# Kernel optimization log

Hardware: AMD Instinct MI355X
Metric: run time of the kernel (lower is better)

The kernel has to match this reference:

```python
import jax, jax.numpy as jnp
import numpy as np
from jax import lax

EPS = 1e-5
S_CENTROIDS = 2048
K_NEIGH = 32


def _fps(xyz, S):
    """Farthest point sampling. xyz: (B,N,3) -> idx (B,S) int32."""
    B, N, _ = xyz.shape

    def body(carry, _):
        dist, farthest = carry  # (B,N), (B,)
        centroid = jnp.take_along_axis(xyz, farthest[:, None, None], axis=1)  # (B,1,3)
        d = jnp.sum((xyz - centroid) ** 2, axis=-1)  # (B,N)
        dist = jnp.minimum(dist, d)
        nxt = jnp.argmax(dist, axis=-1).astype(jnp.int32)
        return (dist, nxt), farthest

    init = (jnp.full((B, N), 1e10, xyz.dtype), jnp.zeros((B,), jnp.int32))
    _, idx = lax.scan(body, init, None, length=S)
    return idx.T  # (B,S)


def _knn(q, p, K):
    """q: (B,S,3) queries, p: (B,N,3) points -> idx (B,S,K) of K nearest."""
    d = (jnp.sum(q * q, -1)[:, :, None] + jnp.sum(p * p, -1)[:, None, :]
         - 2.0 * jnp.einsum('bsd,bnd->bsn', q, p))  # (B,S,N) sq dists
    _, idx = lax.top_k(-d, K)
    return idx


def _mlp_layer(x, w, g, b, m, v):
    # x: (B,S,K,Cin); 1x1 conv == channel matmul, then eval-mode BN, then ReLU
    x = jnp.einsum('bskc,oc->bsko', x, w)
    x = (x - m) * (g * lax.rsqrt(v + EPS)) + b
    return jax.nn.relu(x)


def setup_inputs() -> dict:
    key = jax.random.key(0)
    ks = jax.random.split(key, 8)
    B, N, D = 4, 8192, 64
    inp = {
        'xyz': jax.random.normal(ks[0], (B, N, 3), jnp.float32),
        'points': jax.random.normal(ks[1], (B, D, N), jnp.float32),
        'w0': jax.random.normal(ks[2], (64, 67), jnp.float32) * (1.0 / np.sqrt(67)),
        'g0': jnp.ones((64,), jnp.float32), 'b0': jnp.zeros((64,), jnp.float32),
        'm0': jnp.zeros((64,), jnp.float32), 'v0': jnp.ones((64,), jnp.float32),
        'w1': jax.random.normal(ks[3], (64, 64), jnp.float32) * (1.0 / np.sqrt(64)),
        'g1': jnp.ones((64,), jnp.float32), 'b1': jnp.zeros((64,), jnp.float32),
        'm1': jnp.zeros((64,), jnp.float32), 'v1': jnp.ones((64,), jnp.float32),
        'w2': jax.random.normal(ks[4], (128, 64), jnp.float32) * (1.0 / np.sqrt(64)),
        'g2': jnp.ones((128,), jnp.float32), 'b2': jnp.zeros((128,), jnp.float32),
        'm2': jnp.zeros((128,), jnp.float32), 'v2': jnp.ones((128,), jnp.float32),
    }
    return inp


def reference(xyz, points, w0, g0, b0, m0, v0, w1, g1, b1, m1, v1,
              w2, g2, b2, m2, v2):
    B, N, _ = xyz.shape
    S, K = S_CENTROIDS, K_NEIGH

    # FPS centroids (S < N path of the module)
    fps_idx = _fps(xyz, S)                                        # (B,S)
    new_xyz = jnp.take_along_axis(xyz, fps_idx[..., None], axis=1)  # (B,S,3)

    # KNN grouping
    idx = _knn(new_xyz, xyz, K)                                   # (B,S,K)
    grouped_xyz = jnp.take_along_axis(xyz[:, None], idx[..., None], axis=2)  # (B,S,K,3)
    grouped_xyz = grouped_xyz - new_xyz[:, :, None, :]

    # gather neighbor features: points (B,D,N) -> (B,N,D) -> (B,S,K,D)
    pts = jnp.transpose(points, (0, 2, 1))
    neigh = jnp.take_along_axis(pts[:, None], idx[..., None], axis=2)
    grouped = jnp.concatenate([grouped_xyz, neigh], axis=-1)      # (B,S,K,3+D)

    x = _mlp_layer(grouped, w0, g0, b0, m0, v0)
    x = _mlp_layer(x, w1, g1, b1, m1, v1)
    x = _mlp_layer(x, w2, g2, b2, m2, v2)                         # (B,S,K,128)

    new_points = jnp.transpose(jnp.max(x, axis=2), (0, 2, 1))     # (B,128,S)
    return new_xyz, new_points
```

## Files before the change

### kernel.cpp

```cpp
#include <hip/hip_runtime.h>
#include <cfloat>
#include <climits>

#define NPTS   8192
#define SCENT  2048
#define KNEIGH 32
#define BATCH  4
#define DFEAT  64
#define FPS_T  512
#define NV     8
#define NW     8
#define CAP    64
#define NCONS  252
#define CPB    63

typedef float v2f __attribute__((ext_vector_type(2)));

#define DPPTOP2(um, us, ctrl, rmask)                                                  \
    { unsigned _tm = (unsigned)__builtin_amdgcn_update_dpp(0, (int)(um), (ctrl),      \
                                                           (rmask), 0xf, false);     \
      unsigned _ts = (unsigned)__builtin_amdgcn_update_dpp(0, (int)(us), (ctrl),      \
                                                           (rmask), 0xf, false);     \
      unsigned _lo = ((um) < _tm) ? (um) : _tm;                                       \
      (us) = ((us) > _ts) ? (us) : _ts;                                               \
      (us) = ((us) > _lo) ? (us) : _lo;                                               \
      (um) = ((um) > _tm) ? (um) : _tm; }

#define FLUSH_PUB(Eidx, VX, VY, VZ, HASPREV, PX, PY, PZ)                              \
    if (((Eidx) & 63) == 63) {                                                        \
        const int base0 = (Eidx) - 63;                                                \
        if (t < 64 * 3) {                                                             \
            const int ci = base0 + t / 3;                                             \
            const int cc = t - (t / 3) * 3;                                           \
            float v;                                                                  \
            if (ci == (Eidx))                                                         \
                v = (cc == 0) ? (VX) : ((cc == 1) ? (VY) : (VZ));                     \
            else if ((HASPREV) && ci == (Eidx) - 1)                                   \
                v = (cc == 0) ? (PX) : ((cc == 1) ? (PY) : (PZ));                     \
            else                                                                      \
                v = (cc == 0) ? S.hx[ci] : ((cc == 1) ? S.hy[ci] : S.hz[ci]);         \
            __hip_atomic_store(&new_xyz[((size_t)b * SCENT + base0) * 3 + t], v,      \
                               __ATOMIC_RELAXED, __HIP_MEMORY_SCOPE_AGENT);           \
        }                                                                             \
        __syncthreads();                 \
        if (t == 0)                                                                   \
            __hip_atomic_store(&progress[b], (Eidx) + 1,                              \
                               __ATOMIC_RELEASE, __HIP_MEMORY_SCOPE_AGENT);           \
    }

struct FpsSh {
    float sx[NPTS], sy[NPTS], sz[NPTS];
    float hx[SCENT], hy[SCENT], hz[SCENT];
    alignas(16) unsigned slotQ[2][NW][4];
    int scand[CAP];
    int scnt;
    alignas(8) double sdd[2][NW];
    double sfv[NW];
    int sfo[NW];
};
struct ConsSh {
    float  spx[2048], spy[2048], spz[2048];
    double sp2[2048];
    float  tile[32 * 33];
    float  regA[64 * 68];
    float  regB[64 * 64];
    float  regC[128 * 64];
    float  prm[512];
};
union ShU { FpsSh f; ConsSh c; };

__global__ __launch_bounds__(FPS_T, 1) void fused_kernel(
        const float* __restrict__ xyz, float* __restrict__ new_xyz,
        const float* __restrict__ pts, float* __restrict__ ptsT,
        int* __restrict__ progress, int* __restrict__ tcount,
        float* __restrict__ out_points,
        const float* __restrict__ w0, const float* __restrict__ g0,
        const float* __restrict__ b0, const float* __restrict__ m0,
        const float* __restrict__ v0, const float* __restrict__ w1,
        const float* __restrict__ g1, const float* __restrict__ b1,
        const float* __restrict__ m1, const float* __restrict__ v1,
        const float* __restrict__ w2, const float* __restrict__ g2,
        const float* __restrict__ b2, const float* __restrict__ m2,
        const float* __restrict__ v2) {
    __shared__ ShU sh;
    const int t = threadIdx.x;
    const int lane = t & 63, w = t >> 6;

    if (blockIdx.x < BATCH) {
        FpsSh& S = sh.f;
        const int b = blockIdx.x;
        const float* X = xyz + (size_t)b * NPTS * 3;

        for (int p = t; p < NPTS; p += FPS_T) {
            S.sx[p] = X[3 * p + 0]; S.sy[p] = X[3 * p + 1]; S.sz[p] = X[3 * p + 2];
        }

        v2f px2[NV], py2[NV], pz2[NV], dist2[NV];
#pragma unroll
        for (int j = 0; j < NV; ++j) {
            int pA = t + FPS_T * j, pB = t + FPS_T * (j + NV);
            px2[j] = (v2f){X[3 * pA + 0], X[3 * pB + 0]};
            py2[j] = (v2f){X[3 * pA + 1], X[3 * pB + 1]};
            pz2[j] = (v2f){X[3 * pA + 2], X[3 * pB + 2]};
            dist2[j] = (v2f){1e10f, 1e10f};
        }
        float c0x = X[0], c0y = X[1], c0z = X[2];
        float c1x = 0.f, c1y = 0.f, c1z = 0.f;
        int dual = 0, buf = 0;
        int E = 1;
        if (t == 0) { S.hx[0] = c0x; S.hy[0] = c0y; S.hz[0] = c0z; }
        __syncthreads();

#pragma unroll 1
        while (true) {
            float m2s = -1.f, s2s = -1.f;
            {
                const v2f c0xx = {c0x, c0x}, c0yy = {c0y, c0y}, c0zz = {c0z, c0z};
                if (dual) {
                    const v2f c1xx = {c1x, c1x}, c1yy = {c1y, c1y}, c1zz = {c1z, c1z};
#pragma unroll
                    for (int j = 0; j < NV; ++j) {
                        v2f dx = px2[j] - c0xx, dy = py2[j] - c0yy, dz = pz2[j] - c0zz;
                        v2f d0 = __builtin_elementwise_fma(dx, dx,
                                 __builtin_elementwise_fma(dy, dy, dz * dz));
                        v2f ex = px2[j] - c1xx, ey = py2[j] - c1yy, ez = pz2[j] - c1zz;
                        v2f d1 = __builtin_elementwise_fma(ex, ex,
                                 __builtin_elementwise_fma(ey, ey, ez * ez));
                        v2f d  = __builtin_elementwise_min(d0, d1);
                        v2f nd = __builtin_elementwise_min(dist2[j], d);
                        dist2[j] = nd;
                        float hi = fmaxf(nd.x, nd.y), lo = fminf(nd.x, nd.y);
                        s2s = fmaxf(fmaxf(s2s, lo), fminf(m2s, hi));
                        m2s = fmaxf(m2s, hi);
                    }
                } else {
#pragma unroll
                    for (int j = 0; j < NV; ++j) {
                        v2f dx = px2[j] - c0xx, dy = py2[j] - c0yy, dz = pz2[j] - c0zz;
                        v2f d  = __builtin_elementwise_fma(dx, dx,
                                 __builtin_elementwise_fma(dy, dy, dz * dz));
                        v2f nd = __builtin_elementwise_min(dist2[j], d);
                        dist2[j] = nd;
                        float hi = fmaxf(nd.x, nd.y), lo = fminf(nd.x, nd.y);
                        s2s = fmaxf(fmaxf(s2s, lo), fminf(m2s, hi));
                        m2s = fmaxf(m2s, hi);
                    }
                }
            }
            const float m = m2s, sec = s2s;

            int mi = 0;
#pragma unroll
            for (int j = 0; j < NV; ++j) {
                mi = (dist2[j].x == m) ? (t + FPS_T * j)        : mi;
                mi = (dist2[j].y == m) ? (t + FPS_T * (j + NV)) : mi;
            }

            const unsigned myU = __float_as_uint(m);
            unsigned um = myU, us = __float_as_uint(sec);
            DPPTOP2(um, us, 0x111, 0xf);
            DPPTOP2(um, us, 0x112, 0xf);
            DPPTOP2(um, us, 0x114, 0xf);
            DPPTOP2(um, us, 0x118, 0xf);
            DPPTOP2(um, us, 0x142, 0xa);
            DPPTOP2(um, us, 0x143, 0xc);
            const unsigned wu  = (unsigned)__builtin_amdgcn_readlane((int)um, 63);
            const unsigned wsu = (unsigned)__builtin_amdgcn_readlane((int)us, 63);

            unsigned long long wb = __ballot(myU == wu);
            const int wl   = __ffsll(wb) - 1;
            const int widx = __builtin_amdgcn_readlane(mi, wl);
            const float thwf = __fmul_rn(__uint_as_float(wu), 0.999998f);
            unsigned long long b1m = __ballot(m >= thwf);
            unsigned long long b2m = __ballot(sec >= thwf);
            const unsigned tw = (b2m || __popcll(b1m) >= 2) ? 1u : 0u;
            if (lane == 0) {
                *(uint4*)&S.slotQ[buf][w][0] =
                    make_uint4(wu, (unsigned)widx | (tw << 14), wsu, 0u);
            }
            __syncthreads();

            unsigned mv[NW], mt4[NW], sv2[NW];
            {
                const uint4* qp = (const uint4*)&S.slotQ[buf][0][0];
                uint4 u0 = qp[0], u1 = qp[1], u2 = qp[2], u3 = qp[3];
                uint4 u4 = qp[4], u5 = qp[5], u6 = qp[6], u7 = qp[7];
                mv[0]=u0.x; mt4[0]=u0.y; sv2[0]=u0.z;
                mv[1]=u1.x; mt4[1]=u1.y; sv2[1]=u1.z;
                mv[2]=u2.x; mt4[2]=u2.y; sv2[2]=u2.z;
                mv[3]=u3.x; mt4[3]=u3.y; sv2[3]=u3.z;
                mv[4]=u4.x; mt4[4]=u4.y; sv2[4]=u4.z;
                mv[5]=u5.x; mt4[5]=u5.y; sv2[5]=u5.z;
                mv[6]=u6.x; mt4[6]=u6.y; sv2[6]=u6.z;
                mv[7]=u7.x; mt4[7]=u7.y; sv2[7]=u7.z;
            }
            unsigned gu = mv[0];
#pragma unroll
            for (int k = 1; k < NW; ++k) gu = (mv[k] > gu) ? mv[k] : gu;
            const float gvf  = __uint_as_float(gu);
            const float gthf = __fmul_rn(gvf, 0.999998f);
            const unsigned ugth = __float_as_uint(gthf);
            int nw = 0; unsigned meta = 0; int kw = 0;
#pragma unroll
            for (int k = NW - 1; k >= 0; --k) {
                nw  += (mv[k] >= ugth) ? 1 : 0;
                meta = (mv[k] == gu) ? mt4[k] : meta;
                kw   = (mv[k] == gu) ? k : kw;
            }
            const int wtie = (meta >> 14) & 1;
            int i1 = (int)(meta & 0x3fffu);
            const int fb = (nw >= 2) || wtie;

            if (fb) {
                if (t == 0) S.scnt = 0;
                __syncthreads();
#pragma unroll
                for (int j = 0; j < NV; ++j) {
                    if (dist2[j].x >= gthf) {
                        int slot = atomicAdd(&S.scnt, 1);
                        if (slot < CAP) S.scand[slot] = t + FPS_T * j;
                    }
                    if (dist2[j].y >= gthf) {
                        int slot = atomicAdd(&S.scnt, 1);
                        if (slot < CAP) S.scand[slot] = t + FPS_T * (j + NV);
                    }
                }
                __syncthreads();
                const int mm = S.scnt;
                if (mm <= CAP) {
                    double bd = -1.0; int bi = INT_MAX;
#pragma unroll 1
                    for (int k = 0; k < mm; ++k) {
                        const int pos = S.scand[k];
                        const double pxd = (double)S.sx[pos], pyd = (double)S.sy[pos],
                                     pzd = (double)S.sz[pos];
                        double dd = 1e10;
                        for (int i = t; i < E; i += FPS_T) {
                            double ddx = __dsub_rn(pxd, (double)S.hx[i]);
                            double ddy = __dsub_rn(pyd, (double)S.hy[i]);
                            double ddz = __dsub_rn(pzd, (double)S.hz[i]);
                            double d = __dadd_rn(__dadd_rn(__dmul_rn(ddx, ddx), __dmul_rn(ddy, ddy)),
                                                 __dmul_rn(ddz, ddz));
                            dd = fmin(dd, d);
                        }
#pragma unroll
                        for (int off = 32; off >= 1; off >>= 1)
                            dd = fmin(dd, __shfl_down(dd, off));
                        if (lane == 0) S.sdd[k & 1][w] = dd;
                        __syncthreads();
                        double ddm = S.sdd[k & 1][0];
#pragma unroll
                        for (int w2i = 1; w2i < NW; ++w2i) ddm = fmin(ddm, S.sdd[k & 1][w2i]);
                        if (ddm > bd || (ddm == bd && pos < bi)) { bd = ddm; bi = pos; }
                    }
                    i1 = bi;
                } else {
                    double bv = -1.0; int bi = INT_MAX;
#pragma unroll 1
                    for (int j = 0; j < 2 * NV; ++j) {
                        const int jj = j & (NV - 1);
                        const bool hiHalf = j >= NV;
                        const double pxd = (double)(hiHalf ? px2[jj].y : px2[jj].x);
                        const double pyd = (double)(hiHalf ? py2[jj].y : py2[jj].x);
                        const double pzd = (double)(hiHalf ? pz2[jj].y : pz2[jj].x);
                        double dd = 1e10;
                        for (int i = 0; i < E; ++i) {
                            double ddx = __dsub_rn(pxd, (double)S.hx[i]);
                            double ddy = __dsub_rn(pyd, (double)S.hy[i]);
                            double ddz = __dsub_rn(pzd, (double)S.hz[i]);
                            double d = __dadd_rn(__dadd_rn(__dmul_rn(ddx, ddx), __dmul_rn(ddy, ddy)),
                                                 __dmul_rn(ddz, ddz));
                            dd = fmin(dd, d);
                        }
                        int pidx = t + FPS_T * j;
                        if (dd > bv || (dd == bv && pidx < bi)) { bv = dd; bi = pidx; }
                    }
#pragma unroll
                    for (int off = 32; off >= 1; off >>= 1) {
                        double ov = __shfl_down(bv, off);
                        int    oi = __shfl_down(bi, off);
                        if (ov > bv || (ov == bv && oi < bi)) { bv = ov; bi = oi; }
                    }
                    if (lane == 0) { S.sfv[w] = bv; S.sfo[w] = bi; }
                    __syncthreads();
                    bv = S.sfv[0]; bi = S.sfo[0];
#pragma unroll
                    for (int w2i = 1; w2i < NW; ++w2i) {
                        double ov = S.sfv[w2i]; int oi = S.sfo[w2i];
                        if (ov > bv || (ov == bv && oi < bi)) { bv = ov; bi = oi; }
                    }
                    i1 = bi;
                }
                __syncthreads();
            }

            const float e0x = S.sx[i1], e0y = S.sy[i1], e0z = S.sz[i1];
            if (t == 0) { S.hx[E] = e0x; S.hy[E] = e0y; S.hz[E] = e0z; }
            FLUSH_PUB(E, e0x, e0y, e0z, 0, 0.f, 0.f, 0.f);
            c0x = e0x; c0y = e0y; c0z = e0z;

            int peeled = 0;
            float e1x = 0.f, e1y = 0.f, e1z = 0.f;
            if (!fb && (E + 1) < SCENT) {
                unsigned arr[NW];
#pragma unroll
                for (int k = 0; k < NW; ++k) arr[k] = (k == kw) ? sv2[k] : mv[k];
                unsigned v2u = arr[0];
#pragma unroll
                for (int k = 1; k < NW; ++k) v2u = (arr[k] > v2u) ? arr[k] : v2u;
                int k2 = 0; unsigned meta2 = 0;
#pragma unroll
                for (int k = NW - 1; k >= 0; --k) {
                    meta2 = (arr[k] == v2u) ? mt4[k] : meta2;
                    k2    = (arr[k] == v2u) ? k : k2;
                }
                const float v2vf = __uint_as_float(v2u);
                const unsigned uthr2 = __float_as_uint(__fmul_rn(v2vf, 0.999998f));
                int cnt = 0;
#pragma unroll
                for (int k = 0; k < NW; ++k)
                    cnt += ((mv[k] >= uthr2) ? 1 : 0) + ((sv2[k] >= uthr2) ? 1 : 0);
                const int i2 = (int)(meta2 & 0x3fffu);
                e1x = S.sx[i2]; e1y = S.sy[i2]; e1z = S.sz[i2];
                const float ddx = e1x - e0x, ddy = e1y - e0y, ddz = e1z - e0z;
                const float dq = fmaf(ddx, ddx, fmaf(ddy, ddy, ddz * ddz));
                peeled = ((k2 != kw) && (cnt == 2) &&
                          (dq >= __fmul_rn(v2vf, 1.000002f))) ? 1 : 0;
            }
            if (peeled) {
                const int e1i = E + 1;
                if (t == 0) { S.hx[e1i] = e1x; S.hy[e1i] = e1y; S.hz[e1i] = e1z; }
                FLUSH_PUB(e1i, e1x, e1y, e1z, 1, e0x, e0y, e0z);
                c1x = e1x; c1y = e1y; c1z = e1z;
                dual = 1;
                E = e1i + 1;
            } else {
                dual = 0;
                E = E + 1;
            }
            if (E >= SCENT) break;
            buf ^= 1;
        }
    } else {
        ConsSh& K = sh.c;
        const int local = blockIdx.x - BATCH;
        const int batch = local / CPB;
        const int cl    = local % CPB;
        const int tx = t & 31, ty = t >> 5;

        for (int tid2 = local; tid2 < 2048; tid2 += NCONS) {
            const int bt = tid2 >> 9, rest = tid2 & 511;
            const int d0 = (rest >> 8) * 32, n0 = (rest & 255) * 32;
            __syncthreads();
#pragma unroll
            for (int i = 0; i < 2; ++i)
                K.tile[(ty + 16 * i) * 33 + tx] =
                    pts[(size_t)bt * DFEAT * NPTS + (size_t)(d0 + ty + 16 * i) * NPTS + n0 + tx];
            __syncthreads();
#pragma unroll
            for (int i = 0; i < 2; ++i)
                ptsT[(size_t)bt * NPTS * DFEAT + (size_t)(n0 + ty + 16 * i) * DFEAT + d0 + tx] =
                    K.tile[tx * 33 + ty + 16 * i];
        }
        if (t == 0) {
            __threadfence();
            atomicAdd(tcount, 1);
        }

        for (int idx = t; idx < 64 * 68; idx += FPS_T) {
            int o = idx / 68, i = idx - o * 68;
            float v;
            if (i < 64)      v = w0[o * 67 + 3 + i];
            else if (i < 67) v = w0[o * 67 + (i - 64)];
            else             v = 0.0f;
            K.regA[idx] = v;
        }
        for (int idx = t; idx < 64 * 64; idx += FPS_T)  K.regB[idx] = w1[idx];
        for (int idx = t; idx < 128 * 64; idx += FPS_T) K.regC[idx] = w2[idx];
        if (t < 64) {
            float a0v = g0[t] / sqrtf(v0[t] + 1e-5f);
            K.prm[t]       = a0v;
            K.prm[64 + t]  = b0[t] - m0[t] * a0v;
            float a1v = g1[t] / sqrtf(v1[t] + 1e-5f);
            K.prm[128 + t] = a1v;
            K.prm[192 + t] = b1[t] - m1[t] * a1v;
        } else if (t < 192) {
            int o = t - 64;
            float a2v = g2[o] / sqrtf(v2[o] + 1e-5f);
            K.prm[256 + o] = a2v;
            K.prm[384 + o] = b2[o] - m2[o] * a2v;
        }

        const float* Xb = xyz + (size_t)batch * NPTS * 3;
#pragma unroll 1
        for (int r = 0; ; ++r) {
            const int sBase = r * (CPB * NW) + cl * NW;
            if (sBase >= SCENT) break;
            const int sMax = min(sBase + NW - 1, SCENT - 1);
            if (t == 0) {
                while (__hip_atomic_load(&progress[batch], __ATOMIC_ACQUIRE,
                                         __HIP_MEMORY_SCOPE_AGENT) < sMax + 1)
                    __builtin_amdgcn_s_sleep(8);
                if (r == 0) {
                    while (__hip_atomic_load(tcount, __ATOMIC_ACQUIRE,
                                             __HIP_MEMORY_SCOPE_AGENT) < NCONS)
                        __builtin_amdgcn_s_sleep(8);
                }
            }
            __syncthreads();

            const int sQ = min(sBase + w, SCENT - 1);
            const float* q = new_xyz + ((size_t)batch * SCENT + sQ) * 3;
            const float qfx = q[0], qfy = q[1], qfz = q[2];
            const double qx = (double)qfx, qy = (double)qfy, qz = (double)qfz;
            const double q2 = __dadd_rn(__dadd_rn(__dmul_rn(qx, qx), __dmul_rn(qy, qy)),
                                        __dmul_rn(qz, qz));

            double ld   = DBL_MAX;
            int    li   = 0x7fffffff;
            double taud = DBL_MAX;
            int    taui = 0x7fffffff;

#pragma unroll 1
            for (int c = 0; c < 4; ++c) {
                __syncthreads();
#pragma unroll
                for (int r2 = 0; r2 < 4; ++r2) {
                    int pl = r2 * 512 + t;
                    int p  = c * 2048 + pl;
                    float x = Xb[3 * p + 0], y = Xb[3 * p + 1], z = Xb[3 * p + 2];
                    K.spx[pl] = x; K.spy[pl] = y; K.spz[pl] = z;
                    double dx = (double)x, dy = (double)y, dz = (double)z;
                    K.sp2[pl] = __dadd_rn(__dadd_rn(__dmul_rn(dx, dx), __dmul_rn(dy, dy)),
                                          __dmul_rn(dz, dz));
                }
                __syncthreads();
#pragma unroll 1
                for (int i = 0; i < 32; ++i) {
                    const int pl   = i * 64 + lane;
                    const int pidx = c * 2048 + pl;
                    double px = (double)K.spx[pl], py = (double)K.spy[pl],
                           pz = (double)K.spz[pl];
                    double qp = __dadd_rn(__dadd_rn(__dmul_rn(qx, px), __dmul_rn(qy, py)),
                                          __dmul_rn(qz, pz));
                    double d  = __dsub_rn(__dadd_rn(q2, K.sp2[pl]), __dmul_rn(2.0, qp));
                    bool cand = (d < taud) || (d == taud && pidx < taui);
                    unsigned long long mmask = __ballot(cand);
                    while (mmask) {
                        int sl = __ffsll((unsigned long long)mmask) - 1;
                        mmask &= mmask - 1;
                        double dv = __shfl(d, sl);
                        int    iv = __shfl(pidx, sl);
                        if (dv < taud || (dv == taud && iv < taui)) {
                            bool gt = (lane < 32) && (ld > dv || (ld == dv && li > iv));
                            unsigned long long gm = __ballot(gt);
                            double ud = __shfl_up(ld, 1);
                            int    ui = __shfl_up(li, 1);
                            if (gt) { ld = ud; li = ui; }
                            bool first = gt && ((lane == 0) || !((gm >> (lane - 1)) & 1ull));
                            if (first) { ld = dv; li = iv; }
                            taud = __shfl(ld, 31);
                            taui = __shfl(li, 31);
                        }
                    }
                }
            }

            if (sBase + w < SCENT && lane < 32) {
                const int nidx = li;
                const float* P3 = Xb + (size_t)nidx * 3;
                const float dx = P3[0] - qfx, dy = P3[1] - qfy, dz = P3[2] - qfz;

                const float4* F = (const float4*)(ptsT + ((size_t)batch * NPTS + nidx) * 64);
                float4 xv[17];
#pragma unroll
                for (int i = 0; i < 16; ++i) xv[i] = F[i];
                xv[16] = make_float4(dx, dy, dz, 0.0f);

                float h0[64];
                const float4* W0 = (const float4*)K.regA;
#pragma unroll
                for (int o = 0; o < 64; ++o) {
                    float acc = 0.f;
#pragma unroll
                    for (int i = 0; i < 17; ++i) {
                        float4 ww = W0[o * 17 + i];
                        acc = fmaf(xv[i].x, ww.x, acc);
                        acc = fmaf(xv[i].y, ww.y, acc);
                        acc = fmaf(xv[i].z, ww.z, acc);
                        acc = fmaf(xv[i].w, ww.w, acc);
                    }
                    h0[o] = fmaxf(fmaf(acc, K.prm[o], K.prm[64 + o]), 0.f);
                }
                float h1[64];
                const float4* W1 = (const float4*)K.regB;
#pragma unroll
                for (int o = 0; o < 64; ++o) {
                    float acc = 0.f;
#pragma unroll
                    for (int i = 0; i < 16; ++i) {
                        float4 ww = W1[o * 16 + i];
                        acc = fmaf(h0[4 * i + 0], ww.x, acc);
                        acc = fmaf(h0[4 * i + 1], ww.y, acc);
                        acc = fmaf(h0[4 * i + 2], ww.z, acc);
                        acc = fmaf(h0[4 * i + 3], ww.w, acc);
                    }
                    h1[o] = fmaxf(fmaf(acc, K.prm[128 + o], K.prm[192 + o]), 0.f);
                }
                const float4* W2 = (const float4*)K.regC;
                float* outp = out_points + (size_t)batch * 128 * SCENT + sQ;
#pragma unroll 1
                for (int o = 0; o < 128; ++o) {
                    float acc = 0.f;
#pragma unroll
                    for (int i = 0; i < 16; ++i) {
                        float4 ww = W2[o * 16 + i];
                        acc = fmaf(h1[4 * i + 0], ww.x, acc);
                        acc = fmaf(h1[4 * i + 1], ww.y, acc);
                        acc = fmaf(h1[4 * i + 2], ww.z, acc);
                        acc = fmaf(h1[4 * i + 3], ww.w, acc);
                    }
                    float y = fmaxf(fmaf(acc, K.prm[256 + o], K.prm[384 + o]), 0.f);
#pragma unroll
                    for (int off = 16; off >= 1; off >>= 1)
                        y = fmaxf(y, __shfl_xor(y, off));
                    if (lane == 0) outp[(size_t)o * SCENT] = y;
                }
            }
        }
    }
}

extern "C" void kernel_launch(void* const* d_in, const int* in_sizes, int n_in,
                              void* d_out, int out_size, void* d_ws, size_t ws_size,
                              hipStream_t stream) {
    const float* xyz    = (const float*)d_in[0];
    const float* points = (const float*)d_in[1];
    const float* w0 = (const float*)d_in[2];
    const float* g0 = (const float*)d_in[3];
    const float* b0 = (const float*)d_in[4];
    const float* m0 = (const float*)d_in[5];
    const float* v0 = (const float*)d_in[6];
    const float* w1 = (const float*)d_in[7];
    const float* g1 = (const float*)d_in[8];
    const float* b1 = (const float*)d_in[9];
    const float* m1 = (const float*)d_in[10];
    const float* v1 = (const float*)d_in[11];
    const float* w2 = (const float*)d_in[12];
    const float* g2 = (const float*)d_in[13];
    const float* b2 = (const float*)d_in[14];
    const float* m2 = (const float*)d_in[15];
    const float* v2 = (const float*)d_in[16];

    float* out_xyz    = (float*)d_out;
    float* out_points = (float*)d_out + (size_t)BATCH * SCENT * 3;

    char* ws = (char*)d_ws;
    int*   progress = (int*)ws;
    int*   tcount   = (int*)(ws + 64);
    float* ptsT     = (float*)(ws + 32768);

    hipMemsetAsync(ws, 0, 128, stream);

    void* kargs[] = { (void*)&xyz, (void*)&out_xyz, (void*)&points, (void*)&ptsT,
                      (void*)&progress, (void*)&tcount, (void*)&out_points,
                      (void*)&w0, (void*)&g0, (void*)&b0, (void*)&m0, (void*)&v0,
                      (void*)&w1, (void*)&g1, (void*)&b1, (void*)&m1, (void*)&v1,
                      (void*)&w2, (void*)&g2, (void*)&b2, (void*)&m2, (void*)&v2 };
    hipLaunchCooperativeKernel((const void*)fused_kernel,
                               dim3(BATCH + NCONS), dim3(FPS_T), kargs, 0, stream);
}
```

Baseline: 2.332 ms.

## Process two FPS batches per block, interleaving their iterations to share barriers

The FPS work moves from four blocks (one batch each) to two blocks that each advance two batches in lockstep, so the per-iteration reduction barrier covers both batches and their independent latency chains can overlap. The LDS copy of all points is dropped: candidate coordinates are stored alongside their indices, and winner points are loaded from global memory. Publishing moves from the whole block to a single wave, which waits on its own stores before setting progress, so that flush no longer needs a block-wide barrier. The cost is doubled register pressure for point data in each FPS block and serial dependence of the two batches on the same compute unit. This may lengthen the critical FPS path if the computation per iteration, rather than latency, is what limits speed.

```diff
diff --git a/kernel.cpp b/kernel.cpp
--- a/kernel.cpp
+++ b/kernel.cpp
@@ -11,6 +11,7 @@
 #define NV     8
 #define NW     8
 #define CAP    64
+#define PBLK   2
 #define NCONS  252
 #define CPB    63
 
@@ -26,34 +27,43 @@
       (us) = ((us) > _lo) ? (us) : _lo;                                               \
       (um) = ((um) > _tm) ? (um) : _tm; }
 
-#define FLUSH_PUB(Eidx, VX, VY, VZ, HASPREV, PX, PY, PZ)                              \
+#define ULOAD3(Xp, idx, ox, oy, oz)                                                   \
+    { const int _u = __builtin_amdgcn_readfirstlane(idx);                             \
+      const float* _p = (Xp) + 3 * (size_t)_u;                                        \
+      ox = _p[0]; oy = _p[1]; oz = _p[2]; }
+
+#define FLUSH_Q(qq, gb, Eidx, VX, VY, VZ, HASPREV, PX, PY, PZ)                        \
     if (((Eidx) & 63) == 63) {                                                        \
-        const int base0 = (Eidx) - 63;                                                \
-        if (t < 64 * 3) {                                                             \
-            const int ci = base0 + t / 3;                                             \
-            const int cc = t - (t / 3) * 3;                                           \
-            float v;                                                                  \
-            if (ci == (Eidx))                                                         \
-                v = (cc == 0) ? (VX) : ((cc == 1) ? (VY) : (VZ));                     \
-            else if ((HASPREV) && ci == (Eidx) - 1)                                   \
-                v = (cc == 0) ? (PX) : ((cc == 1) ? (PY) : (PZ));                     \
-            else                                                                      \
-                v = (cc == 0) ? S.hx[ci] : ((cc == 1) ? S.hy[ci] : S.hz[ci]);         \
-            __hip_atomic_store(&new_xyz[((size_t)b * SCENT + base0) * 3 + t], v,      \
-                               __ATOMIC_RELAXED, __HIP_MEMORY_SCOPE_AGENT);           \
+        if (w == (qq)) {                                                              \
+            const int base0 = (Eidx) - 63;                                            \
+            for (int rep = 0; rep < 3; ++rep) {                                       \
+                const int li = rep * 64 + lane;                                       \
+                const int ci = base0 + li / 3;                                        \
+                const int cc = li - (li / 3) * 3;                                     \
+                float v;                                                              \
+                if (ci == (Eidx))                                                     \
+                    v = (cc == 0) ? (VX) : ((cc == 1) ? (VY) : (VZ));                 \
+                else if ((HASPREV) && ci == (Eidx) - 1)                               \
+                    v = (cc == 0) ? (PX) : ((cc == 1) ? (PY) : (PZ));                 \
+                else                                                                  \
+                    v = (cc == 0) ? S.hx[qq][ci]                                      \
+                                  : ((cc == 1) ? S.hy[qq][ci] : S.hz[qq][ci]);        \
+                __hip_atomic_store(&new_xyz[((size_t)(gb) * SCENT + base0) * 3 + li], \
+                                   v, __ATOMIC_RELAXED, __HIP_MEMORY_SCOPE_AGENT);    \
+            }                                                                         \
+            asm volatile("s_waitcnt vmcnt(0)" ::: "memory");                          \
+            if (lane == 0)                                                            \
+                __hip_atomic_store(&progress[gb], (Eidx) + 1,                         \
+                                   __ATOMIC_RELEASE, __HIP_MEMORY_SCOPE_AGENT);       \
         }                                                                             \
-        __syncthreads();                 \
-        if (t == 0)                                                                   \
-            __hip_atomic_store(&progress[b], (Eidx) + 1,                              \
-                               __ATOMIC_RELEASE, __HIP_MEMORY_SCOPE_AGENT);           \
     }
 
 struct FpsSh {
-    float sx[NPTS], sy[NPTS], sz[NPTS];
-    float hx[SCENT], hy[SCENT], hz[SCENT];
-    alignas(16) unsigned slotQ[2][NW][4];
-    int scand[CAP];
-    int scnt;
+    float hx[2][SCENT], hy[2][SCENT], hz[2][SCENT];
+    alignas(16) unsigned slotQ[2][2][NW][4];
+    float scandX[CAP], scandY[CAP], scandZ[CAP];
+    int   scandI[CAP];
+    int   scnt;
     alignas(8) double sdd[2][NW];
     double sfv[NW];
     int sfo[NW];
@@ -86,264 +96,295 @@
     const int t = threadIdx.x;
     const int lane = t & 63, w = t >> 6;
 
-    if (blockIdx.x < BATCH) {
+    if (blockIdx.x < PBLK) {
         FpsSh& S = sh.f;
-        const int b = blockIdx.x;
-        const float* X = xyz + (size_t)b * NPTS * 3;
-
-        for (int p = t; p < NPTS; p += FPS_T) {
-            S.sx[p] = X[3 * p + 0]; S.sy[p] = X[3 * p + 1]; S.sz[p] = X[3 * p + 2];
-        }
-
-        v2f px2[NV], py2[NV], pz2[NV], dist2[NV];
+        const int bA = blockIdx.x * 2;
+        const float* XA = xyz + (size_t)bA * NPTS * 3;
+        const float* XB = xyz + (size_t)(bA + 1) * NPTS * 3;
+
+        v2f px2[2][NV], py2[2][NV], pz2[2][NV], dist2[2][NV];
 #pragma unroll
         for (int j = 0; j < NV; ++j) {
-            int pA = t + FPS_T * j, pB = t + FPS_T * (j + NV);
-            px2[j] = (v2f){X[3 * pA + 0], X[3 * pB + 0]};
-            py2[j] = (v2f){X[3 * pA + 1], X[3 * pB + 1]};
-            pz2[j] = (v2f){X[3 * pA + 2], X[3 * pB + 2]};
-            dist2[j] = (v2f){1e10f, 1e10f};
-        }
-        float c0x = X[0], c0y = X[1], c0z = X[2];
-        float c1x = 0.f, c1y = 0.f, c1z = 0.f;
-        int dual = 0, buf = 0;
-        int E = 1;
-        if (t == 0) { S.hx[0] = c0x; S.hy[0] = c0y; S.hz[0] = c0z; }
+            const int pA = t + FPS_T * j, pB = t + FPS_T * (j + NV);
+            px2[0][j] = (v2f){XA[3 * pA + 0], XA[3 * pB + 0]};
+            py2[0][j] = (v2f){XA[3 * pA + 1], XA[3 * pB + 1]};
+            pz2[0][j] = (v2f){XA[3 * pA + 2], XA[3 * pB + 2]};
+            px2[1][j] = (v2f){XB[3 * pA + 0], XB[3 * pB + 0]};
+            py2[1][j] = (v2f){XB[3 * pA + 1], XB[3 * pB + 1]};
+            pz2[1][j] = (v2f){XB[3 * pA + 2], XB[3 * pB + 2]};
+            dist2[0][j] = (v2f){1e10f, 1e10f};
+            dist2[1][j] = (v2f){1e10f, 1e10f};
+        }
+        float c0x[2] = {XA[0], XB[0]}, c0y[2] = {XA[1], XB[1]}, c0z[2] = {XA[2], XB[2]};
+        float c1x[2] = {0.f, 0.f}, c1y[2] = {0.f, 0.f}, c1z[2] = {0.f, 0.f};
+        int dual[2] = {0, 0};
+        int E[2] = {1, 1};
+        if (t == 0) {
+            S.hx[0][0] = c0x[0]; S.hy[0][0] = c0y[0]; S.hz[0][0] = c0z[0];
+            S.hx[1][0] = c0x[1]; S.hy[1][0] = c0y[1]; S.hz[1][0] = c0z[1];
+        }
+        int buf = 0;
         __syncthreads();
 
 #pragma unroll 1
-        while (true) {
-            float m2s = -1.f, s2s = -1.f;
-            {
-                const v2f c0xx = {c0x, c0x}, c0yy = {c0y, c0y}, c0zz = {c0z, c0z};
-                if (dual) {
-                    const v2f c1xx = {c1x, c1x}, c1yy = {c1y, c1y}, c1zz = {c1z, c1z};
-#pragma unroll
-                    for (int j = 0; j < NV; ++j) {
-                        v2f dx = px2[j] - c0xx, dy = py2[j] - c0yy, dz = pz2[j] - c0zz;
-                        v2f d0 = __builtin_elementwise_fma(dx, dx,
-                                 __builtin_elementwise_fma(dy, dy, dz * dz));
-                        v2f ex = px2[j] - c1xx, ey = py2[j] - c1yy, ez = pz2[j] - c1zz;
-                        v2f d1 = __builtin_elementwise_fma(ex, ex,
-                                 __builtin_elementwise_fma(ey, ey, ez * ez));
-                        v2f d  = __builtin_elementwise_min(d0, d1);
-                        v2f nd = __builtin_elementwise_min(dist2[j], d);
-                        dist2[j] = nd;
-                        float hi = fmaxf(nd.x, nd.y), lo = fminf(nd.x, nd.y);
-                        s2s = fmaxf(fmaxf(s2s, lo), fminf(m2s, hi));
-                        m2s = fmaxf(m2s, hi);
-                    }
-                } else {
-#pragma unroll
-                    for (int j = 0; j < NV; ++j) {
-                        v2f dx = px2[j] - c0xx, dy = py2[j] - c0yy, dz = pz2[j] - c0zz;
-                        v2f d  = __builtin_elementwise_fma(dx, dx,
-                                 __builtin_elementwise_fma(dy, dy, dz * dz));
-                        v2f nd = __builtin_elementwise_min(dist2[j], d);
-                        dist2[j] = nd;
-                        float hi = fmaxf(nd.x, nd.y), lo = fminf(nd.x, nd.y);
-                        s2s = fmaxf(fmaxf(s2s, lo), fminf(m2s, hi));
-                        m2s = fmaxf(m2s, hi);
-                    }
-                }
-            }
-            const float m = m2s, sec = s2s;
-
-            int mi = 0;
-#pragma unroll
-            for (int j = 0; j < NV; ++j) {
-                mi = (dist2[j].x == m) ? (t + FPS_T * j)        : mi;
-                mi = (dist2[j].y == m) ? (t + FPS_T * (j + NV)) : mi;
-            }
-
-            const unsigned myU = __float_as_uint(m);
-            unsigned um = myU, us = __float_as_uint(sec);
-            DPPTOP2(um, us, 0x111, 0xf);
-            DPPTOP2(um, us, 0x112, 0xf);
-            DPPTOP2(um, us, 0x114, 0xf);
-            DPPTOP2(um, us, 0x118, 0xf);
-            DPPTOP2(um, us, 0x142, 0xa);
-            DPPTOP2(um, us, 0x143, 0xc);
-            const unsigned wu  = (unsigned)__builtin_amdgcn_readlane((int)um, 63);
-            const unsigned wsu = (unsigned)__builtin_amdgcn_readlane((int)us, 63);
-
-            unsigned long long wb = __ballot(myU == wu);
-            const int wl   = __ffsll(wb) - 1;
-            const int widx = __builtin_amdgcn_readlane(mi, wl);
-            const float thwf = __fmul_rn(__uint_as_float(wu), 0.999998f);
-            unsigned long long b1m = __ballot(m >= thwf);
-            unsigned long long b2m = __ballot(sec >= thwf);
-            const unsigned tw = (b2m || __popcll(b1m) >= 2) ? 1u : 0u;
-            if (lane == 0) {
-                *(uint4*)&S.slotQ[buf][w][0] =
-                    make_uint4(wu, (unsigned)widx | (tw << 14), wsu, 0u);
+        while (E[0] < SCENT || E[1] < SCENT) {
+#pragma unroll
+            for (int q = 0; q < 2; ++q) if (E[q] < SCENT) {
+                float m2s = -1.f, s2s = -1.f;
+                {
+                    const v2f cxx = {c0x[q], c0x[q]}, cyy = {c0y[q], c0y[q]},
+                              czz = {c0z[q], c0z[q]};
+                    if (dual[q]) {
+                        const v2f exx = {c1x[q], c1x[q]}, eyy = {c1y[q], c1y[q]},
+                                  ezz = {c1z[q], c1z[q]};
+#pragma unroll
+                        for (int j = 0; j < NV; ++j) {
+                            v2f dx = px2[q][j] - cxx, dy = py2[q][j] - cyy,
+                                dz = pz2[q][j] - czz;
+                            v2f d0 = __builtin_elementwise_fma(dx, dx,
+                                     __builtin_elementwise_fma(dy, dy, dz * dz));
+                            v2f ex = px2[q][j] - exx, ey = py2[q][j] - eyy,
+                                ez = pz2[q][j] - ezz;
+                            v2f d1 = __builtin_elementwise_fma(ex, ex,
+                                     __builtin_elementwise_fma(ey, ey, ez * ez));
+                            v2f d  = __builtin_elementwise_min(d0, d1);
+                            v2f nd = __builtin_elementwise_min(dist2[q][j], d);
+                            dist2[q][j] = nd;
+                            float hi = fmaxf(nd.x, nd.y), lo = fminf(nd.x, nd.y);
+                            s2s = fmaxf(fmaxf(s2s, lo), fminf(m2s, hi));
+                            m2s = fmaxf(m2s, hi);
+                        }
+                    } else {
+#pragma unroll
+                        for (int j = 0; j < NV; ++j) {
+                            v2f dx = px2[q][j] - cxx, dy = py2[q][j] - cyy,
+                                dz = pz2[q][j] - czz;
+                            v2f d  = __builtin_elementwise_fma(dx, dx,
+                                     __builtin_elementwise_fma(dy, dy, dz * dz));
+                            v2f nd = __builtin_elementwise_min(dist2[q][j], d);
+                            dist2[q][j] = nd;
+                            float hi = fmaxf(nd.x, nd.y), lo = fminf(nd.x, nd.y);
+                            s2s = fmaxf(fmaxf(s2s, lo), fminf(m2s, hi));
+                            m2s = fmaxf(m2s, hi);
+                        }
+                    }
+                }
+                const float m = m2s, sec = s2s;
+
+                int mi = 0;
+#pragma unroll
+                for (int j = 0; j < NV; ++j) {
+                    mi = (dist2[q][j].x == m) ? (t + FPS_T * j)        : mi;
+                    mi = (dist2[q][j].y == m) ? (t + FPS_T * (j + NV)) : mi;
+                }
+
+                const unsigned myU = __float_as_uint(m);
+                unsigned um = myU, us = __float_as_uint(sec);
+                DPPTOP2(um, us, 0x111, 0xf);
+                DPPTOP2(um, us, 0x112, 0xf);
+                DPPTOP2(um, us, 0x114, 0xf);
+                DPPTOP2(um, us, 0x118, 0xf);
+                DPPTOP2(um, us, 0x142, 0xa);
+                DPPTOP2(um, us, 0x143, 0xc);
+                const unsigned wu  = (unsigned)__builtin_amdgcn_readlane((int)um, 63);
+                const unsigned wsu = (unsigned)__builtin_amdgcn_readlane((int)us, 63);
+
+                unsigned long long wb = __ballot(myU == wu);
+                const int wl   = __ffsll(wb) - 1;
+                const int widx = __builtin_amdgcn_readlane(mi, wl);
+                const float thwf = __fmul_rn(__uint_as_float(wu), 0.999998f);
+                unsigned long long b1m = __ballot(m >= thwf);
+                unsigned long long b2m = __ballot(sec >= thwf);
+                const unsigned tw = (b2m || __popcll(b1m) >= 2) ? 1u : 0u;
+                if (lane == 0) {
+                    *(uint4*)&S.slotQ[q][buf][w][0] =
+                        make_uint4(wu, (unsigned)widx | (tw << 14), wsu, 0u);
+                }
             }
             __syncthreads();
 
-            unsigned mv[NW], mt4[NW], sv2[NW];
-            {
-                const uint4* qp = (const uint4*)&S.slotQ[buf][0][0];
-                uint4 u0 = qp[0], u1 = qp[1], u2 = qp[2], u3 = qp[3];
-                uint4 u4 = qp[4], u5 = qp[5], u6 = qp[6], u7 = qp[7];
-                mv[0]=u0.x; mt4[0]=u0.y; sv2[0]=u0.z;
-                mv[1]=u1.x; mt4[1]=u1.y; sv2[1]=u1.z;
-                mv[2]=u2.x; mt4[2]=u2.y; sv2[2]=u2.z;
-                mv[3]=u3.x; mt4[3]=u3.y; sv2[3]=u3.z;
-                mv[4]=u4.x; mt4[4]=u4.y; sv2[4]=u4.z;
-                mv[5]=u5.x; mt4[5]=u5.y; sv2[5]=u5.z;
-                mv[6]=u6.x; mt4[6]=u6.y; sv2[6]=u6.z;
-                mv[7]=u7.x; mt4[7]=u7.y; sv2[7]=u7.z;
+#pragma unroll
+            for (int q = 0; q < 2; ++q) if (E[q] < SCENT) {
+                const float* __restrict__ Xq = q ? XB : XA;
+                const int gb = bA + q;
+
+                unsigned mv[NW], mt4[NW], sv2[NW];
+#pragma unroll
+                for (int k = 0; k < NW; ++k) {
+                    const uint4 u = *(const uint4*)&S.slotQ[q][buf][k][0];
+                    mv[k] = u.x; mt4[k] = u.y; sv2[k] = u.z;
+                }
+                unsigned gu = mv[0];
+#pragma unroll
+                for (int k = 1; k < NW; ++k) gu = (mv[k] > gu) ? mv[k] : gu;
+                const float gvf  = __uint_as_float(gu);
+                const float gthf = __fmul_rn(gvf, 0.999998f);
+                const unsigned ugth = __float_as_uint(gthf);
+                int nw = 0; unsigned meta = 0; int kw = 0;
+#pragma unroll
+                for (int k = NW - 1; k >= 0; --k) {
+                    nw  += (mv[k] >= ugth) ? 1 : 0;
+                    meta = (mv[k] == gu) ? mt4[k] : meta;
+                    kw   = (mv[k] == gu) ? k : kw;
+                }
+                const int wtie = (meta >> 14) & 1;
+                int i1 = (int)(meta & 0x3fffu);
+                const int fb = (nw >= 2) || wtie;
+
+                float e0x, e0y, e0z;
+                if (fb) {
+                    if (t == 0) S.scnt = 0;
+                    __syncthreads();
+#pragma unroll
+                    for (int j = 0; j < NV; ++j) {
+                        if (dist2[q][j].x >= gthf) {
+                            int slot = atomicAdd(&S.scnt, 1);
+                            if (slot < CAP) {
+                                S.scandX[slot] = px2[q][j].x; S.scandY[slot] = py2[q][j].x;
+                                S.scandZ[slot] = pz2[q][j].x; S.scandI[slot] = t + FPS_T * j;
+                            }
+                        }
+                        if (dist2[q][j].y >= gthf) {
+                            int slot = atomicAdd(&S.scnt, 1);
+                            if (slot < CAP) {
+                                S.scandX[slot] = px2[q][j].y; S.scandY[slot] = py2[q][j].y;
+                                S.scandZ[slot] = pz2[q][j].y;
+                                S.scandI[slot] = t + FPS_T * (j + NV);
+                            }
+                        }
+                    }
+                    __syncthreads();
+                    const int mm = S.scnt;
+                    if (mm <= CAP) {
+                        double bd = -1.0; int bi = INT_MAX;
+                        float bx = 0.f, by = 0.f, bz = 0.f;
+#pragma unroll 1
+                        for (int k = 0; k < mm; ++k) {
+                            const float fx = S.scandX[k], fy = S.scandY[k], fz = S.scandZ[k];
+                            const int   fi = S.scandI[k];
+                            const double pxd = (double)fx, pyd = (double)fy,
+                                         pzd = (double)fz;
+                            double dd = 1e10;
+                            for (int i = t; i < E[q]; i += FPS_T) {
+                                double ddx = __dsub_rn(pxd, (double)S.hx[q][i]);
+                                double ddy = __dsub_rn(pyd, (double)S.hy[q][i]);
+                                double ddz = __dsub_rn(pzd, (double)S.hz[q][i]);
+                                double d = __dadd_rn(__dadd_rn(__dmul_rn(ddx, ddx),
+                                                               __dmul_rn(ddy, ddy)),
+                                                     __dmul_rn(ddz, ddz));
+                                dd = fmin(dd, d);
+                            }
+#pragma unroll
+                            for (int off = 32; off >= 1; off >>= 1)
+                                dd = fmin(dd, __shfl_down(dd, off));
+                            if (lane == 0) S.sdd[k & 1][w] = dd;
+                            __syncthreads();
+                            double ddm = S.sdd[k & 1][0];
+#pragma unroll
+                            for (int w2i = 1; w2i < NW; ++w2i)
+                                ddm = fmin(ddm, S.sdd[k & 1][w2i]);
+                            if (ddm > bd || (ddm == bd && fi < bi)) {
+                                bd = ddm; bi = fi; bx = fx; by = fy; bz = fz;
+                            }
+                        }
+                        i1 = bi; e0x = bx; e0y = by; e0z = bz;
+                    } else {
+                        double bv = -1.0; int bi = INT_MAX;
+#pragma unroll 1
+                        for (int j = 0; j < 2 * NV; ++j) {
+                            const int pidx = t + FPS_T * j;
+                            const double pxd = (double)Xq[3 * pidx + 0];
+                            const double pyd = (double)Xq[3 * pidx + 1];
+                            const double pzd = (double)Xq[3 * pidx + 2];
+                            double dd = 1e10;
+                            for (int i = 0; i < E[q]; ++i) {
+                                double ddx = __dsub_rn(pxd, (double)S.hx[q][i]);
+                                double ddy = __dsub_rn(pyd, (double)S.hy[q][i]);
+                                double ddz = __dsub_rn(pzd, (double)S.hz[q][i]);
+                                double d = __dadd_rn(__dadd_rn(__dmul_rn(ddx, ddx),
+                                                               __dmul_rn(ddy, ddy)),
+                                                     __dmul_rn(ddz, ddz));
+                                dd = fmin(dd, d);
+                            }
+                            if (dd > bv || (dd == bv && pidx < bi)) { bv = dd; bi = pidx; }
+                        }
+#pragma unroll
+                        for (int off = 32; off >= 1; off >>= 1) {
+                            double ov = __shfl_down(bv, off);
+                            int    oi = __shfl_down(bi, off);
+                            if (ov > bv || (ov == bv && oi < bi)) { bv = ov; bi = oi; }
+                        }
+                        if (lane == 0) { S.sfv[w] = bv; S.sfo[w] = bi; }
+                        __syncthreads();
+                        bv = S.sfv[0]; bi = S.sfo[0];
+#pragma unroll
+                        for (int w2i = 1; w2i < NW; ++w2i) {
+                            double ov = S.sfv[w2i]; int oi = S.sfo[w2i];
+                            if (ov > bv || (ov == bv && oi < bi)) { bv = ov; bi = oi; }
+                        }
+                        i1 = bi;
+                        ULOAD3(Xq, i1, e0x, e0y, e0z);
+                    }
+                    __syncthreads();
+                } else {
+                    ULOAD3(Xq, i1, e0x, e0y, e0z);
+                }
+
+                if (t == 0) {
+                    S.hx[q][E[q]] = e0x; S.hy[q][E[q]] = e0y; S.hz[q][E[q]] = e0z;
+                }
+
+                int peeled = 0;
+                float e1x = 0.f, e1y = 0.f, e1z = 0.f;
+                if (!fb && (E[q] + 1) < SCENT) {
+                    unsigned arr[NW];
+#pragma unroll
+                    for (int k = 0; k < NW; ++k) arr[k] = (k == kw) ? sv2[k] : mv[k];
+                    unsigned v2u = arr[0];
+#pragma unroll
+                    for (int k = 1; k < NW; ++k) v2u = (arr[k] > v2u) ? arr[k] : v2u;
+                    int k2 = 0; unsigned meta2 = 0;
+#pragma unroll
+                    for (int k = NW - 1; k >= 0; --k) {
+                        meta2 = (arr[k] == v2u) ? mt4[k] : meta2;
+                        k2    = (arr[k] == v2u) ? k : k2;
+                    }
+                    const float v2vf = __uint_as_float(v2u);
+                    const unsigned uthr2 = __float_as_uint(__fmul_rn(v2vf, 0.999998f));
+                    int cnt = 0;
+#pragma unroll
+                    for (int k = 0; k < NW; ++k)
+                        cnt += ((mv[k] >= uthr2) ? 1 : 0) + ((sv2[k] >= uthr2) ? 1 : 0);
+                    const int i2 = (int)(meta2 & 0x3fffu);
+                    ULOAD3(Xq, i2, e1x, e1y, e1z);
+                    const float ddx = e1x - e0x, ddy = e1y - e0y, ddz = e1z - e0z;
+                    const float dq = fmaf(ddx, ddx, fmaf(ddy, ddy, ddz * ddz));
+                    peeled = ((k2 != kw) && (cnt == 2) &&
+                              (dq >= __fmul_rn(v2vf, 1.000002f))) ? 1 : 0;
+                }
+
+                FLUSH_Q(q, gb, E[q], e0x, e0y, e0z, 0, 0.f, 0.f, 0.f);
+                c0x[q] = e0x; c0y[q] = e0y; c0z[q] = e0z;
+
+                if (peeled) {
+                    const int e1i = E[q] + 1;
+                    if (t == 0) {
+                        S.hx[q][e1i] = e1x; S.hy[q][e1i] = e1y; S.hz[q][e1i] = e1z;
+                    }
+                    FLUSH_Q(q, gb, e1i, e1x, e1y, e1z, 1, e0x, e0y, e0z);
+                    c1x[q] = e1x; c1y[q] = e1y; c1z[q] = e1z;
+                    dual[q] = 1;
+                    E[q] = e1i + 1;
+                } else {
+                    dual[q] = 0;
+                    E[q] = E[q] + 1;
+                }
             }
-            unsigned gu = mv[0];
-#pragma unroll
-            for (int k = 1; k < NW; ++k) gu = (mv[k] > gu) ? mv[k] : gu;
-            const float gvf  = __uint_as_float(gu);
-            const float gthf = __fmul_rn(gvf, 0.999998f);
-            const unsigned ugth = __float_as_uint(gthf);
-            int nw = 0; unsigned meta = 0; int kw = 0;
-#pragma unroll
-            for (int k = NW - 1; k >= 0; --k) {
-                nw  += (mv[k] >= ugth) ? 1 : 0;
-                meta = (mv[k] == gu) ? mt4[k] : meta;
-                kw   = (mv[k] == gu) ? k : kw;
-            }
-            const int wtie = (meta >> 14) & 1;
-            int i1 = (int)(meta & 0x3fffu);
-            const int fb = (nw >= 2) || wtie;
-
-            if (fb) {
-                if (t == 0) S.scnt = 0;
-                __syncthreads();
-#pragma unroll
-                for (int j = 0; j < NV; ++j) {
-                    if (dist2[j].x >= gthf) {
-                        int slot = atomicAdd(&S.scnt, 1);
-                        if (slot < CAP) S.scand[slot] = t + FPS_T * j;
-                    }
-                    if (dist2[j].y >= gthf) {
-                        int slot = atomicAdd(&S.scnt, 1);
-                        if (slot < CAP) S.scand[slot] = t + FPS_T * (j + NV);
-                    }
-                }
-                __syncthreads();
-                const int mm = S.scnt;
-                if (mm <= CAP) {
-                    double bd = -1.0; int bi = INT_MAX;
-#pragma unroll 1
-                    for (int k = 0; k < mm; ++k) {
-                        const int pos = S.scand[k];
-                        const double pxd = (double)S.sx[pos], pyd = (double)S.sy[pos],
-                                     pzd = (double)S.sz[pos];
-                        double dd = 1e10;
-                        for (int i = t; i < E; i += FPS_T) {
-                            double ddx = __dsub_rn(pxd, (double)S.hx[i]);
-                            double ddy = __dsub_rn(pyd, (double)S.hy[i]);
-                            double ddz = __dsub_rn(pzd, (double)S.hz[i]);
-                            double d = __dadd_rn(__dadd_rn(__dmul_rn(ddx, ddx), __dmul_rn(ddy, ddy)),
-                                                 __dmul_rn(ddz, ddz));
-                            dd = fmin(dd, d);
-                        }
-#pragma unroll
-                        for (int off = 32; off >= 1; off >>= 1)
-                            dd = fmin(dd, __shfl_down(dd, off));
-                        if (lane == 0) S.sdd[k & 1][w] = dd;
-                        __syncthreads();
-                        double ddm = S.sdd[k & 1][0];
-#pragma unroll
-                        for (int w2i = 1; w2i < NW; ++w2i) ddm = fmin(ddm, S.sdd[k & 1][w2i]);
-                        if (ddm > bd || (ddm == bd && pos < bi)) { bd = ddm; bi = pos; }
-                    }
-                    i1 = bi;
-                } else {
-                    double bv = -1.0; int bi = INT_MAX;
-#pragma unroll 1
-                    for (int j = 0; j < 2 * NV; ++j) {
-                        const int jj = j & (NV - 1);
-                        const bool hiHalf = j >= NV;
-                        const double pxd = (double)(hiHalf ? px2[jj].y : px2[jj].x);
-                        const double pyd = (double)(hiHalf ? py2[jj].y : py2[jj].x);
-                        const double pzd = (double)(hiHalf ? pz2[jj].y : pz2[jj].x);
-                        double dd = 1e10;
-                        for (int i = 0; i < E; ++i) {
-                            double ddx = __dsub_rn(pxd, (double)S.hx[i]);
-                            double ddy = __dsub_rn(pyd, (double)S.hy[i]);
-                            double ddz = __dsub_rn(pzd, (double)S.hz[i]);
-                            double d = __dadd_rn(__dadd_rn(__dmul_rn(ddx, ddx), __dmul_rn(ddy, ddy)),
-                                                 __dmul_rn(ddz, ddz));
-                            dd = fmin(dd, d);
-                        }
-                        int pidx = t + FPS_T * j;
-                        if (dd > bv || (dd == bv && pidx < bi)) { bv = dd; bi = pidx; }
-                    }
-#pragma unroll
-                    for (int off = 32; off >= 1; off >>= 1) {
-                        double ov = __shfl_down(bv, off);
-                        int    oi = __shfl_down(bi, off);
-                        if (ov > bv || (ov == bv && oi < bi)) { bv = ov; bi = oi; }
-                    }
-                    if (lane == 0) { S.sfv[w] = bv; S.sfo[w] = bi; }
-                    __syncthreads();
-                    bv = S.sfv[0]; bi = S.sfo[0];
-#pragma unroll
-                    for (int w2i = 1; w2i < NW; ++w2i) {
-                        double ov = S.sfv[w2i]; int oi = S.sfo[w2i];
-                        if (ov > bv || (ov == bv && oi < bi)) { bv = ov; bi = oi; }
-                    }
-                    i1 = bi;
-                }
-                __syncthreads();
-            }
-
-            const float e0x = S.sx[i1], e0y = S.sy[i1], e0z = S.sz[i1];
-            if (t == 0) { S.hx[E] = e0x; S.hy[E] = e0y; S.hz[E] = e0z; }
-            FLUSH_PUB(E, e0x, e0y, e0z, 0, 0.f, 0.f, 0.f);
-            c0x = e0x; c0y = e0y; c0z = e0z;
-
-            int peeled = 0;
-            float e1x = 0.f, e1y = 0.f, e1z = 0.f;
-            if (!fb && (E + 1) < SCENT) {
-                unsigned arr[NW];
-#pragma unroll
-                for (int k = 0; k < NW; ++k) arr[k] = (k == kw) ? sv2[k] : mv[k];
-                unsigned v2u = arr[0];
-#pragma unroll
-                for (int k = 1; k < NW; ++k) v2u = (arr[k] > v2u) ? arr[k] : v2u;
-                int k2 = 0; unsigned meta2 = 0;
-#pragma unroll
-                for (int k = NW - 1; k >= 0; --k) {
-                    meta2 = (arr[k] == v2u) ? mt4[k] : meta2;
-                    k2    = (arr[k] == v2u) ? k : k2;
-                }
-                const float v2vf = __uint_as_float(v2u);
-                const unsigned uthr2 = __float_as_uint(__fmul_rn(v2vf, 0.999998f));
-                int cnt = 0;
-#pragma unroll
-                for (int k = 0; k < NW; ++k)
-                    cnt += ((mv[k] >= uthr2) ? 1 : 0) + ((sv2[k] >= uthr2) ? 1 : 0);
-                const int i2 = (int)(meta2 & 0x3fffu);
-                e1x = S.sx[i2]; e1y = S.sy[i2]; e1z = S.sz[i2];
-                const float ddx = e1x - e0x, ddy = e1y - e0y, ddz = e1z - e0z;
-                const float dq = fmaf(ddx, ddx, fmaf(ddy, ddy, ddz * ddz));
-                peeled = ((k2 != kw) && (cnt == 2) &&
-                          (dq >= __fmul_rn(v2vf, 1.000002f))) ? 1 : 0;
-            }
-            if (peeled) {
-                const int e1i = E + 1;
-                if (t == 0) { S.hx[e1i] = e1x; S.hy[e1i] = e1y; S.hz[e1i] = e1z; }
-                FLUSH_PUB(e1i, e1x, e1y, e1z, 1, e0x, e0y, e0z);
-                c1x = e1x; c1y = e1y; c1z = e1z;
-                dual = 1;
-                E = e1i + 1;
-            } else {
-                dual = 0;
-                E = E + 1;
-            }
-            if (E >= SCENT) break;
             buf ^= 1;
         }
     } else {
         ConsSh& K = sh.c;
-        const int local = blockIdx.x - BATCH;
+        const int local = blockIdx.x - PBLK;
         const int batch = local / CPB;
         const int cl    = local % CPB;
         const int tx = t & 31, ty = t >> 5;
@@ -568,5 +609,5 @@
                       (void*)&w1, (void*)&g1, (void*)&b1, (void*)&m1, (void*)&v1,
                       (void*)&w2, (void*)&g2, (void*)&b2, (void*)&m2, (void*)&v2 };
     hipLaunchCooperativeKernel((const void*)fused_kernel,
-                               dim3(BATCH + NCONS), dim3(FPS_T), kargs, 0, stream);
+                               dim3(PBLK + NCONS), dim3(FPS_T), kargs, 0, stream);
 }
```

New measurement: 6.913 ms. +196.4%, slower.
